# Kernel tuning notes

Hardware: AMD Instinct MI355X
Metric: run time of the kernel (lower is better)

Reference implementation:

```python
import jax, jax.numpy as jnp
import numpy as np

N_NODES = 100000
N_EDGES = 3200000
D = 256


def setup_inputs() -> dict:
    key = jax.random.key(0)
    k1, k2, k3, k4, k5, k6 = jax.random.split(key, 6)
    embeddings = jax.random.normal(k1, (N_NODES, D), dtype=jnp.float32)
    edge_vals = jax.random.uniform(k2, (N_EDGES,), dtype=jnp.float32)
    # glorot-ish scale for the dense transforms
    scale = 1.0 / np.sqrt(D)
    W1 = jax.random.normal(k3, (D, D), dtype=jnp.float32) * scale
    W2 = jax.random.normal(k4, (D, D), dtype=jnp.float32) * scale
    edge_rows = jax.random.randint(k5, (N_EDGES,), 0, N_NODES, dtype=jnp.int32)
    edge_cols = jax.random.randint(k6, (N_EDGES,), 0, N_NODES, dtype=jnp.int32)
    return {
        "embeddings": embeddings,
        "edge_vals": edge_vals,
        "W1": W1,
        "W2": W2,
        "edge_rows": edge_rows,
        "edge_cols": edge_cols,
    }


def reference(embeddings, edge_vals, W1, W2, edge_rows, edge_cols):
    # SpMM: neighbor_interaction = A @ embeddings, A given as COO (rows, cols, vals)
    gathered = edge_vals[:, None] * embeddings[edge_cols]          # [E, D]
    neighbor = jax.ops.segment_sum(gathered, edge_rows,
                                   num_segments=embeddings.shape[0])  # [N, D]
    # include_self_messages = True branch:
    # self_interaction + neighbor_messages  ==  (emb + neighbor) @ W1
    out = (embeddings + neighbor) @ W1 + (neighbor * embeddings) @ W2
    return out
```

## Files before the change

kernel.cpp:

```cpp
#include <hip/hip_runtime.h>
#include <cstdint>
#include <cstddef>

#define N_NODES 100000
#define N_EDGES 3200000
#define DD 256
#define KK 512
#define MPAD 100096
#define NSCAN 98
#define NGRP 8
#define GRP_ROWS 12500
#define NSLOT 256
#define SLOT_E 12500

typedef __attribute__((ext_vector_type(8))) __bf16 bf16x8;
typedef __attribute__((ext_vector_type(4))) __bf16 bf16x4;
typedef __attribute__((ext_vector_type(4))) float f32x4;

__device__ __forceinline__ void gload_lds16(const void* gsrc, void* lds) {
  __builtin_amdgcn_global_load_lds((const __attribute__((address_space(1))) void*)gsrc,
                                   (__attribute__((address_space(3))) void*)lds,
                                   16, 0, 0);
}


__global__ void conve_kernel(const float* __restrict__ emb, __bf16* __restrict__ embB) {
  int i = blockIdx.x * blockDim.x + threadIdx.x;
  float4 v = ((const float4*)emb)[i];
  bf16x4 o;
  o[0] = (__bf16)v.x; o[1] = (__bf16)v.y; o[2] = (__bf16)v.z; o[3] = (__bf16)v.w;
  ((bf16x4*)embB)[i] = o;
}

__global__ void convw_kernel(const float* __restrict__ W1, const float* __restrict__ W2,
                             __bf16* __restrict__ Wt) {
  int idx = blockIdx.x * blockDim.x + threadIdx.x;
  int n = idx >> 9;
  int k = idx & 511;
  float v = (k < 256) ? W1[k * 256 + n] : W2[(k - 256) * 256 + n];
  Wt[idx] = (__bf16)v;
}


__global__ void zero_ints_kernel(int* __restrict__ p, int n) {
  int i = blockIdx.x * blockDim.x + threadIdx.x;
  if (i < n) p[i] = 0;
}

__global__ void hist_kernel(const int* __restrict__ rows, int* __restrict__ counts, int e) {
  int i = blockIdx.x * blockDim.x + threadIdx.x;
  int stride = gridDim.x * blockDim.x;
  for (; i < e; i += stride) atomicAdd(&counts[rows[i]], 1);
}

__global__ void scan_block_kernel(const int* __restrict__ counts, int* __restrict__ offsets,
                                  int* __restrict__ blockSums, int n) {
  __shared__ int s[1024];
  int t = threadIdx.x;
  int i = blockIdx.x * 1024 + t;
  int v = (i < n) ? counts[i] : 0;
  s[t] = v;
  __syncthreads();
  for (int off = 1; off < 1024; off <<= 1) {
    int x = (t >= off) ? s[t - off] : 0;
    __syncthreads();
    s[t] += x;
    __syncthreads();
  }
  if (i < n) offsets[i + 1] = s[t];
  if (t == 1023) blockSums[blockIdx.x] = s[1023];
}

__global__ void scan_sums_kernel(const int* __restrict__ blockSums, int* __restrict__ blockBase,
                                 int nb, int* __restrict__ offsets) {
  __shared__ int s[128];
  int t = threadIdx.x;
  int v = (t < nb) ? blockSums[t] : 0;
  s[t] = v;
  __syncthreads();
  for (int off = 1; off < 128; off <<= 1) {
    int x = (t >= off) ? s[t - off] : 0;
    __syncthreads();
    s[t] += x;
    __syncthreads();
  }
  if (t < nb) blockBase[t] = s[t] - v;
  if (t == 0) offsets[0] = 0;
}

__global__ void scan_add_kernel(const int* __restrict__ counts, int* __restrict__ offsets,
                                const int* __restrict__ blockBase, int* __restrict__ cursor, int n) {
  int i = blockIdx.x * 1024 + threadIdx.x;
  if (i < n) {
    int incl = offsets[i + 1] + blockBase[blockIdx.x];
    offsets[i + 1] = incl;
    cursor[i] = incl - counts[i];
  }
}

__global__ void bin_kernel(const int* __restrict__ rows, const int* __restrict__ cols,
                           const float* __restrict__ vals, int* __restrict__ cursor,
                           uint2* __restrict__ sedge) {
  const int g = blockIdx.x & (NGRP - 1);
  const int s = blockIdx.x >> 3;
  const int rlo = g * GRP_ROWS;
  const int rhi = rlo + GRP_ROWS;
  const int base = s * SLOT_E;
  for (int i = base + threadIdx.x; i < base + SLOT_E; i += 256) {
    int r = rows[i];
    if (r >= rlo && r < rhi) {
      int pos = atomicAdd(&cursor[r], 1);
      sedge[pos] = make_uint2((unsigned)cols[i], __float_as_uint(vals[i]));
    }
  }
}


__global__ void spmm_fuse_kernel(const __bf16* __restrict__ embB, const int* __restrict__ offsets,
                                 const uint2* __restrict__ sedge, __bf16* __restrict__ X) {
  int gw = (blockIdx.x << 2) + (threadIdx.x >> 6);
  int lane = threadIdx.x & 63;
  bf16x4* xp1 = (bf16x4*)(X + (size_t)gw * KK + 4 * lane);
  bf16x4* xp2 = (bf16x4*)(X + (size_t)gw * KK + DD + 4 * lane);
  if (gw >= N_NODES) {
    bf16x4 z;
    z[0] = (__bf16)0.f; z[1] = (__bf16)0.f; z[2] = (__bf16)0.f; z[3] = (__bf16)0.f;
    *xp1 = z; *xp2 = z;
    return;
  }
  const bf16x4* ev = (const bf16x4*)embB;
  float ax = 0.f, ay = 0.f, az = 0.f, aw = 0.f;
  int e = offsets[gw];
  const int eend = offsets[gw + 1];
  for (; e + 3 < eend; e += 4) {
    uint2 e0 = sedge[e], e1 = sedge[e + 1], e2 = sedge[e + 2], e3 = sedge[e + 3];
    float v0 = __uint_as_float(e0.y), v1 = __uint_as_float(e1.y);
    float v2 = __uint_as_float(e2.y), v3 = __uint_as_float(e3.y);
    bf16x4 x0 = ev[(size_t)e0.x * 64 + lane];
    bf16x4 x1 = ev[(size_t)e1.x * 64 + lane];
    bf16x4 x2 = ev[(size_t)e2.x * 64 + lane];
    bf16x4 x3 = ev[(size_t)e3.x * 64 + lane];
    ax = fmaf(v0, (float)x0[0], ax); ay = fmaf(v0, (float)x0[1], ay);
    az = fmaf(v0, (float)x0[2], az); aw = fmaf(v0, (float)x0[3], aw);
    ax = fmaf(v1, (float)x1[0], ax); ay = fmaf(v1, (float)x1[1], ay);
    az = fmaf(v1, (float)x1[2], az); aw = fmaf(v1, (float)x1[3], aw);
    ax = fmaf(v2, (float)x2[0], ax); ay = fmaf(v2, (float)x2[1], ay);
    az = fmaf(v2, (float)x2[2], az); aw = fmaf(v2, (float)x2[3], aw);
    ax = fmaf(v3, (float)x3[0], ax); ay = fmaf(v3, (float)x3[1], ay);
    az = fmaf(v3, (float)x3[2], az); aw = fmaf(v3, (float)x3[3], aw);
  }
  for (; e < eend; ++e) {
    uint2 ee = sedge[e];
    float v = __uint_as_float(ee.y);
    bf16x4 x = ev[(size_t)ee.x * 64 + lane];
    ax = fmaf(v, (float)x[0], ax); ay = fmaf(v, (float)x[1], ay);
    az = fmaf(v, (float)x[2], az); aw = fmaf(v, (float)x[3], aw);
  }
  bf16x4 er = ev[(size_t)gw * 64 + lane];
  float ex = (float)er[0], ey = (float)er[1], ez = (float)er[2], ew = (float)er[3];
  bf16x4 o1, o2;
  o1[0] = (__bf16)(ex + ax); o1[1] = (__bf16)(ey + ay);
  o1[2] = (__bf16)(ez + az); o1[3] = (__bf16)(ew + aw);
  o2[0] = (__bf16)(ex * ax); o2[1] = (__bf16)(ey * ay);
  o2[2] = (__bf16)(ez * az); o2[3] = (__bf16)(ew * aw);
  *xp1 = o1;
  *xp2 = o2;
}


__global__ __launch_bounds__(256) void gemm_kernel(const __bf16* __restrict__ X,
                                                   const __bf16* __restrict__ Wt,
                                                   float* __restrict__ out) {
  __shared__ __align__(16) __bf16 As[128 * 64];
  __shared__ __align__(16) __bf16 Bs[128 * 64];
  const int t = threadIdx.x;
  const int w = t >> 6, lane = t & 63;
  const int m0 = blockIdx.x * 128;
  const int n0 = blockIdx.y * 128;
  const int wm = (w >> 1) * 64, wn = (w & 1) * 64;
  const int lrow = lane >> 3, lcol = lane & 7;

  f32x4 acc[4][4];
#pragma unroll
  for (int i = 0; i < 4; ++i)
#pragma unroll
    for (int j = 0; j < 4; ++j) {
      f32x4 z = {0.f, 0.f, 0.f, 0.f};
      acc[i][j] = z;
    }

  for (int kt = 0; kt < KK; kt += 64) {
#pragma unroll
    for (int q = 0; q < 4; ++q) {
      const int cbase = w * 256 + q * 64;
      const int arow = m0 + w * 32 + q * 8 + lrow;
      gload_lds16(X + (size_t)arow * KK + kt + lcol * 8, (char*)As + cbase * 16);
      const int brow = n0 + w * 32 + q * 8 + lrow;
      gload_lds16(Wt + (size_t)brow * KK + kt + lcol * 8, (char*)Bs + cbase * 16);
    }
    __syncthreads();
#pragma unroll
    for (int kk = 0; kk < 64; kk += 32) {
      const int ko = kk + (lane >> 4) * 8;
      bf16x8 af[4], bg[4];
#pragma unroll
      for (int i = 0; i < 4; ++i)
        af[i] = *(const bf16x8*)(As + (wm + i * 16 + (lane & 15)) * 64 + ko);
#pragma unroll
      for (int j = 0; j < 4; ++j)
        bg[j] = *(const bf16x8*)(Bs + (wn + j * 16 + (lane & 15)) * 64 + ko);
#pragma unroll
      for (int i = 0; i < 4; ++i)
#pragma unroll
        for (int j = 0; j < 4; ++j)
          acc[i][j] = __builtin_amdgcn_mfma_f32_16x16x32_bf16(af[i], bg[j], acc[i][j], 0, 0, 0);
    }
    __syncthreads();
  }

  const int orow0 = m0 + wm + ((lane >> 4) << 2);
  const int ocol0 = n0 + wn + (lane & 15);
#pragma unroll
  for (int i = 0; i < 4; ++i)
#pragma unroll
    for (int j = 0; j < 4; ++j)
#pragma unroll
      for (int r = 0; r < 4; ++r) {
        const int row = orow0 + i * 16 + r;
        if (row < N_NODES) out[(size_t)row * DD + ocol0 + j * 16] = acc[i][j][r];
      }
}


extern "C" void kernel_launch(void* const* d_in, const int* in_sizes, int n_in,
                              void* d_out, int out_size, void* d_ws, size_t ws_size,
                              hipStream_t stream) {
  const float* emb  = (const float*)d_in[0];
  const float* ev   = (const float*)d_in[1];
  const float* W1   = (const float*)d_in[2];
  const float* W2   = (const float*)d_in[3];
  const int* erows  = (const int*)d_in[4];
  const int* ecols  = (const int*)d_in[5];
  float* out = (float*)d_out;
  char* ws = (char*)d_ws;

  const size_t OFF_X   = 0;
  const size_t OFF_EMB = OFF_X   + (size_t)MPAD * KK * 2;
  const size_t OFF_WT  = OFF_EMB + (size_t)N_NODES * DD * 2;
  const size_t OFF_CNT = OFF_WT  + (size_t)KK * DD * 2;
  const size_t OFF_OFS = OFF_CNT + 401408;
  const size_t OFF_CUR = OFF_OFS + 401408;
  const size_t OFF_BS  = OFF_CUR + 401408;
  const size_t OFF_BB  = OFF_BS  + 4096;
  const size_t OFF_SE  = OFF_BB  + 4096;

  __bf16* X     = (__bf16*)(ws + OFF_X);
  __bf16* embB  = (__bf16*)(ws + OFF_EMB);
  __bf16* Wt    = (__bf16*)(ws + OFF_WT);
  int* counts   = (int*)(ws + OFF_CNT);
  int* offsets  = (int*)(ws + OFF_OFS);
  int* cursor   = (int*)(ws + OFF_CUR);
  int* bsums    = (int*)(ws + OFF_BS);
  int* bbase    = (int*)(ws + OFF_BB);
  uint2* sedge  = (uint2*)(ws + OFF_SE);

  conve_kernel<<<(N_NODES * 64) / 256, 256, 0, stream>>>(emb, embB);
  convw_kernel<<<(KK * DD) / 256, 256, 0, stream>>>(W1, W2, Wt);

  zero_ints_kernel<<<(N_NODES + 255) / 256, 256, 0, stream>>>(counts, N_NODES);
  hist_kernel<<<2048, 256, 0, stream>>>(erows, counts, N_EDGES);
  scan_block_kernel<<<NSCAN, 1024, 0, stream>>>(counts, offsets, bsums, N_NODES);
  scan_sums_kernel<<<1, 128, 0, stream>>>(bsums, bbase, NSCAN, offsets);
  scan_add_kernel<<<NSCAN, 1024, 0, stream>>>(counts, offsets, bbase, cursor, N_NODES);
  bin_kernel<<<NGRP * NSLOT, 256, 0, stream>>>(erows, ecols, ev, cursor, sedge);

  spmm_fuse_kernel<<<MPAD / 4, 256, 0, stream>>>(embB, offsets, sedge, X);

  gemm_kernel<<<dim3(MPAD / 128, 2), 256, 0, stream>>>(X, Wt, out);

  (void)in_sizes; (void)n_in; (void)out_size; (void)ws_size;
}
```

Baseline: 770.5 us.

## Group-partition histogram, deepen SpMM gather unroll, swizzle GEMM LDS tiles

The histogram kernel now mirrors the binning kernel's layout: each block scans one slot of edges and counts only rows in its row group, so atomics from one group land in a narrower address range. The cost is that every edge row index is read eight times. The SpMM gather loop is unrolled to eight edges, with all loads issued before the FMAs, to keep more random gathers in flight. The GEMM applies an XOR swizzle to the LDS tile layout, both on the global-to-LDS copy and on the fragment reads, to avoid LDS bank conflicts.

```diff
diff --git a/kernel.cpp b/kernel.cpp
--- a/kernel.cpp
+++ b/kernel.cpp
@@ -47,10 +47,16 @@
   if (i < n) p[i] = 0;
 }
 
-__global__ void hist_kernel(const int* __restrict__ rows, int* __restrict__ counts, int e) {
-  int i = blockIdx.x * blockDim.x + threadIdx.x;
-  int stride = gridDim.x * blockDim.x;
-  for (; i < e; i += stride) atomicAdd(&counts[rows[i]], 1);
+__global__ void hist_kernel(const int* __restrict__ rows, int* __restrict__ counts) {
+  const int g = blockIdx.x & (NGRP - 1);
+  const int s = blockIdx.x >> 3;
+  const int rlo = g * GRP_ROWS;
+  const int rhi = rlo + GRP_ROWS;
+  const int base = s * SLOT_E;
+  for (int i = base + threadIdx.x; i < base + SLOT_E; i += 256) {
+    int r = rows[i];
+    if (r >= rlo && r < rhi) atomicAdd(&counts[r], 1);
+  }
 }
 
 __global__ void scan_block_kernel(const int* __restrict__ counts, int* __restrict__ offsets,
@@ -132,22 +138,33 @@
   float ax = 0.f, ay = 0.f, az = 0.f, aw = 0.f;
   int e = offsets[gw];
   const int eend = offsets[gw + 1];
+  for (; e + 7 < eend; e += 8) {
+    uint2 ee[8];
+    bf16x4 xx[8];
+#pragma unroll
+    for (int u = 0; u < 8; ++u) ee[u] = sedge[e + u];
+#pragma unroll
+    for (int u = 0; u < 8; ++u) xx[u] = ev[(size_t)ee[u].x * 64 + lane];
+#pragma unroll
+    for (int u = 0; u < 8; ++u) {
+      float v = __uint_as_float(ee[u].y);
+      ax = fmaf(v, (float)xx[u][0], ax); ay = fmaf(v, (float)xx[u][1], ay);
+      az = fmaf(v, (float)xx[u][2], az); aw = fmaf(v, (float)xx[u][3], aw);
+    }
+  }
   for (; e + 3 < eend; e += 4) {
-    uint2 e0 = sedge[e], e1 = sedge[e + 1], e2 = sedge[e + 2], e3 = sedge[e + 3];
-    float v0 = __uint_as_float(e0.y), v1 = __uint_as_float(e1.y);
-    float v2 = __uint_as_float(e2.y), v3 = __uint_as_float(e3.y);
-    bf16x4 x0 = ev[(size_t)e0.x * 64 + lane];
-    bf16x4 x1 = ev[(size_t)e1.x * 64 + lane];
-    bf16x4 x2 = ev[(size_t)e2.x * 64 + lane];
-    bf16x4 x3 = ev[(size_t)e3.x * 64 + lane];
-    ax = fmaf(v0, (float)x0[0], ax); ay = fmaf(v0, (float)x0[1], ay);
-    az = fmaf(v0, (float)x0[2], az); aw = fmaf(v0, (float)x0[3], aw);
-    ax = fmaf(v1, (float)x1[0], ax); ay = fmaf(v1, (float)x1[1], ay);
-    az = fmaf(v1, (float)x1[2], az); aw = fmaf(v1, (float)x1[3], aw);
-    ax = fmaf(v2, (float)x2[0], ax); ay = fmaf(v2, (float)x2[1], ay);
-    az = fmaf(v2, (float)x2[2], az); aw = fmaf(v2, (float)x2[3], aw);
-    ax = fmaf(v3, (float)x3[0], ax); ay = fmaf(v3, (float)x3[1], ay);
-    az = fmaf(v3, (float)x3[2], az); aw = fmaf(v3, (float)x3[3], aw);
+    uint2 ee[4];
+    bf16x4 xx[4];
+#pragma unroll
+    for (int u = 0; u < 4; ++u) ee[u] = sedge[e + u];
+#pragma unroll
+    for (int u = 0; u < 4; ++u) xx[u] = ev[(size_t)ee[u].x * 64 + lane];
+#pragma unroll
+    for (int u = 0; u < 4; ++u) {
+      float v = __uint_as_float(ee[u].y);
+      ax = fmaf(v, (float)xx[u][0], ax); ay = fmaf(v, (float)xx[u][1], ay);
+      az = fmaf(v, (float)xx[u][2], az); aw = fmaf(v, (float)xx[u][3], aw);
+    }
   }
   for (; e < eend; ++e) {
     uint2 ee = sedge[e];
@@ -179,6 +196,7 @@
   const int n0 = blockIdx.y * 128;
   const int wm = (w >> 1) * 64, wn = (w & 1) * 64;
   const int lrow = lane >> 3, lcol = lane & 7;
+  const int scol = (lcol ^ lrow) * 8;
 
   f32x4 acc[4][4];
 #pragma unroll
@@ -194,21 +212,27 @@
     for (int q = 0; q < 4; ++q) {
       const int cbase = w * 256 + q * 64;
       const int arow = m0 + w * 32 + q * 8 + lrow;
-      gload_lds16(X + (size_t)arow * KK + kt + lcol * 8, (char*)As + cbase * 16);
+      gload_lds16(X + (size_t)arow * KK + kt + scol, (char*)As + cbase * 16);
       const int brow = n0 + w * 32 + q * 8 + lrow;
-      gload_lds16(Wt + (size_t)brow * KK + kt + lcol * 8, (char*)Bs + cbase * 16);
-    }
-    __syncthreads();
+      gload_lds16(Wt + (size_t)brow * KK + kt + scol, (char*)Bs + cbase * 16);
+    }
+    __syncthreads();
+    const int l15 = lane & 15, lhi = lane >> 4;
 #pragma unroll
     for (int kk = 0; kk < 64; kk += 32) {
-      const int ko = kk + (lane >> 4) * 8;
       bf16x8 af[4], bg[4];
 #pragma unroll
-      for (int i = 0; i < 4; ++i)
-        af[i] = *(const bf16x8*)(As + (wm + i * 16 + (lane & 15)) * 64 + ko);
-#pragma unroll
-      for (int j = 0; j < 4; ++j)
-        bg[j] = *(const bf16x8*)(Bs + (wn + j * 16 + (lane & 15)) * 64 + ko);
+      for (int i = 0; i < 4; ++i) {
+        const int ar = wm + i * 16 + l15;
+        af[i] = *(const bf16x8*)((const char*)As + ar * 128 +
+                                 (((kk + lhi * 8) * 2) ^ ((ar & 7) << 4)));
+      }
+#pragma unroll
+      for (int j = 0; j < 4; ++j) {
+        const int br = wn + j * 16 + l15;
+        bg[j] = *(const bf16x8*)((const char*)Bs + br * 128 +
+                                 (((kk + lhi * 8) * 2) ^ ((br & 7) << 4)));
+      }
 #pragma unroll
       for (int i = 0; i < 4; ++i)
 #pragma unroll
@@ -268,7 +292,7 @@
   convw_kernel<<<(KK * DD) / 256, 256, 0, stream>>>(W1, W2, Wt);
 
   zero_ints_kernel<<<(N_NODES + 255) / 256, 256, 0, stream>>>(counts, N_NODES);
-  hist_kernel<<<2048, 256, 0, stream>>>(erows, counts, N_EDGES);
+  hist_kernel<<<NGRP * NSLOT, 256, 0, stream>>>(erows, counts);
   scan_block_kernel<<<NSCAN, 1024, 0, stream>>>(counts, offsets, bsums, N_NODES);
   scan_sums_kernel<<<1, 128, 0, stream>>>(bsums, bbase, NSCAN, offsets);
   scan_add_kernel<<<NSCAN, 1024, 0, stream>>>(counts, offsets, bbase, cursor, N_NODES);
```

After: 766.7 us. Within noise of the previous version (-0.5%).
